# Performance work log

Hardware: AMD Instinct MI355X
Metric: run time of the kernel (lower is better)

Reference implementation:

```python
import jax, jax.numpy as jnp
import numpy as np

B, C, H, W = 8, 16, 512, 512


def setup_inputs() -> dict:
    key = jax.random.key(0)
    k1, k2, k3 = jax.random.split(key, 3)
    v = jax.random.normal(k1, (B, C, H, W), dtype=jnp.float32)
    # query coords in pixel units, slightly outside [0, W) / [0, H) to hit the invalid mask
    xq = jax.random.uniform(k2, (B, H, W), dtype=jnp.float32) * (W + 2.0) - 1.0
    yq = jax.random.uniform(k3, (B, H, W), dtype=jnp.float32) * (H + 2.0) - 1.0
    return {"v": v, "xq": xq, "yq": yq}


def reference(v, xq, yq):
    b, c, h, w = v.shape
    x0 = jnp.clip(jnp.floor(xq).astype(jnp.int32), 0, w - 1)
    y0 = jnp.clip(jnp.floor(yq).astype(jnp.int32), 0, h - 1)
    x1 = jnp.clip(x0 + 1, 0, w - 1)
    y1 = jnp.clip(y0 + 1, 0, h - 1)

    # flatten v to (B*H*W, C) like _bchw2bhwc(...).view(-1, C)
    v_flat = jnp.transpose(v, (0, 2, 3, 1)).reshape(-1, c)
    offs = (jnp.arange(b, dtype=jnp.int32) * (h * w))[:, None, None]  # [B,1,1]

    def gather(ys, xs):
        idx = (ys * w + xs + offs).reshape(-1)
        return jnp.take(v_flat, idx, axis=0).reshape(b, h, w, c)

    v00 = gather(y0, x0)
    v01 = gather(y0, x1)
    v10 = gather(y1, x0)
    v11 = gather(y1, x1)

    dx = xq - x0.astype(xq.dtype)  # [B,H,W]
    dy = yq - y0.astype(yq.dtype)
    w00 = ((1.0 - dy) * (1.0 - dx))[..., None]
    w01 = ((1.0 - dy) * dx)[..., None]
    w10 = (dy * (1.0 - dx))[..., None]
    w11 = (dy * dx)[..., None]

    out_bhwc = v00 * w00 + v01 * w01 + v10 * w10 + v11 * w11  # [B,H,W,C]
    values = jnp.transpose(out_bhwc, (0, 3, 1, 2))  # [B,C,H,W]

    invalid = ((xq < 0) | (xq >= w) | (yq < 0) | (yq >= h))[:, None, :, :]
    inv = invalid.astype(values.dtype)
    return inv * jnp.zeros_like(values) + (1.0 - inv) * values
```

## Files before the change

kernel.cpp:

```cpp
#include <hip/hip_runtime.h>
#include <hip/hip_fp16.h>


#define BATCH 8
#define CHAN  16
#define HEIGHT 512
#define WIDTH  512
#define HW (HEIGHT * WIDTH)
#define BLOCKS_PER_BATCH (HW / 256)

__global__ __launch_bounds__(256) void transpose_split_f16(
    const float* __restrict__ v, __half* __restrict__ vt0, __half* __restrict__ vt1)
{
    const int blk = blockIdx.x;
    const int b = blk & 7;
    const int j = blk >> 3;
    const int p = j * 256 + threadIdx.x;
    const int tid = b * HW + p;

    const float* src = v + (size_t)b * CHAN * HW + p;

    __half2 d[8];
#pragma unroll
    for (int j2 = 0; j2 < 8; ++j2) {
        const float lo = __builtin_nontemporal_load(&src[(size_t)(2 * j2 + 0) * HW]);
        const float hi = __builtin_nontemporal_load(&src[(size_t)(2 * j2 + 1) * HW]);
        d[j2] = __floats2half2_rn(lo, hi);
    }

    *(uint4*)(vt0 + (size_t)tid * 8) = *(const uint4*)&d[0];
    *(uint4*)(vt1 + (size_t)tid * 8) = *(const uint4*)&d[4];
}

__global__ __launch_bounds__(256) void interp2_half8(
    const __half* __restrict__ vth,
    const float* __restrict__ xq,
    const float* __restrict__ yq,
    float* __restrict__ out,
    int c0)
{
    const int blk = blockIdx.x;
    const int b = blk & 7;
    const int j = blk >> 3;
    const int p = j * 256 + threadIdx.x;
    const int qidx = b * HW + p;

    const float xqv = __builtin_nontemporal_load(&xq[qidx]);
    const float yqv = __builtin_nontemporal_load(&yq[qidx]);

    const bool invalid = (xqv < 0.0f) | (xqv >= (float)WIDTH) |
                         (yqv < 0.0f) | (yqv >= (float)HEIGHT);

    int x0 = (int)floorf(xqv);
    int y0 = (int)floorf(yqv);
    x0 = min(max(x0, 0), WIDTH - 1);
    y0 = min(max(y0, 0), HEIGHT - 1);
    const int x1 = min(x0 + 1, WIDTH - 1);
    const int y1 = min(y0 + 1, HEIGHT - 1);

    const float dx = xqv - (float)x0;
    const float dy = yqv - (float)y0;

    float w00 = (1.0f - dy) * (1.0f - dx);
    float w01 = (1.0f - dy) * dx;
    float w10 = dy * (1.0f - dx);
    float w11 = dy * dx;
    if (invalid) { w00 = 0.0f; w01 = 0.0f; w10 = 0.0f; w11 = 0.0f; }

    const size_t bbase = (size_t)b * HW;

    float acc[8];
#pragma unroll
    for (int c = 0; c < 8; ++c) acc[c] = 0.0f;

    auto corner = [&](int y, int x, float w) {
        const uint4 a = *(const uint4*)(vth + (bbase + (size_t)y * WIDTH + x) * 8);
        const __half2* h = (const __half2*)&a;
#pragma unroll
        for (int k = 0; k < 4; ++k) {
            const float2 f = __half22float2(h[k]);
            acc[2 * k + 0] += w * f.x;
            acc[2 * k + 1] += w * f.y;
        }
    };

    corner(y0, x0, w00);
    corner(y0, x1, w01);
    corner(y1, x0, w10);
    corner(y1, x1, w11);

    const size_t obase = (size_t)b * CHAN * HW + (size_t)c0 * HW + p;
#pragma unroll
    for (int c = 0; c < 8; ++c)
        __builtin_nontemporal_store(acc[c], &out[obase + (size_t)c * HW]);
}

__global__ __launch_bounds__(256) void interp2_bchw(
    const float* __restrict__ v,
    const float* __restrict__ xq,
    const float* __restrict__ yq,
    float* __restrict__ out)
{
    const int tid = blockIdx.x * blockDim.x + threadIdx.x;
    if (tid >= BATCH * HW) return;

    const int b   = tid / HW;
    const int pix = tid - b * HW;

    const float xqv = xq[tid];
    const float yqv = yq[tid];
    const bool invalid = (xqv < 0.0f) | (xqv >= (float)WIDTH) |
                         (yqv < 0.0f) | (yqv >= (float)HEIGHT);

    int x0 = (int)floorf(xqv);
    int y0 = (int)floorf(yqv);
    x0 = min(max(x0, 0), WIDTH - 1);
    y0 = min(max(y0, 0), HEIGHT - 1);
    const int x1 = min(x0 + 1, WIDTH - 1);
    const int y1 = min(y0 + 1, HEIGHT - 1);

    const float dx = xqv - (float)x0;
    const float dy = yqv - (float)y0;
    float w00 = (1.0f - dy) * (1.0f - dx);
    float w01 = (1.0f - dy) * dx;
    float w10 = dy * (1.0f - dx);
    float w11 = dy * dx;
    if (invalid) { w00 = 0.0f; w01 = 0.0f; w10 = 0.0f; w11 = 0.0f; }

    const int off00 = y0 * WIDTH + x0;
    const int off01 = y0 * WIDTH + x1;
    const int off10 = y1 * WIDTH + x0;
    const int off11 = y1 * WIDTH + x1;

    const int vbase = b * CHAN * HW;
    const int obase = vbase + pix;
#pragma unroll
    for (int c = 0; c < CHAN; ++c) {
        const int cb = vbase + c * HW;
        out[obase + c * HW] = v[cb + off00] * w00 + v[cb + off01] * w01 +
                              v[cb + off10] * w10 + v[cb + off11] * w11;
    }
}

extern "C" void kernel_launch(void* const* d_in, const int* in_sizes, int n_in,
                              void* d_out, int out_size, void* d_ws, size_t ws_size,
                              hipStream_t stream) {
    const float* v  = (const float*)d_in[0];
    const float* xq = (const float*)d_in[1];
    const float* yq = (const float*)d_in[2];
    float* out = (float*)d_out;

    const int grid = BATCH * BLOCKS_PER_BATCH;
    const size_t half_bytes = (size_t)BATCH * HW * 8 * sizeof(__half);

    if (ws_size >= 2 * half_bytes) {
        __half* vt0 = (__half*)d_ws;
        __half* vt1 = (__half*)((char*)d_ws + half_bytes);
        transpose_split_f16<<<grid, 256, 0, stream>>>(v, vt0, vt1);
        interp2_half8<<<grid, 256, 0, stream>>>(vt0, xq, yq, out, 0);
        interp2_half8<<<grid, 256, 0, stream>>>(vt1, xq, yq, out, 8);
    } else {
        const int npix = BATCH * HW;
        interp2_bchw<<<(npix + 255) / 256, 256, 0, stream>>>(v, xq, yq, out);
    }
}
```

Measured before the change: 134.7 us.

## Split fp16 transposed volume into four 4-channel planes with paired-pixel row loads

The transposed fp16 copy is now split into four planes of 4 channels each (8 bytes per pixel) instead of two planes of 8 channels. Each interp kernel fetches the two horizontally adjacent pixels of a row with one 16-byte load, clamping the left x so the pair stays in bounds and picking the right halves with selects. This halves the number of gather loads per corner pair and shrinks the per-plane footprint so it caches better. In exchange there are four interp launches instead of two, and xq/yq and the weights are recomputed in each of them.

```diff
diff --git a/kernel.cpp b/kernel.cpp
--- a/kernel.cpp
+++ b/kernel.cpp
@@ -7,33 +7,44 @@
 #define HEIGHT 512
 #define WIDTH  512
 #define HW (HEIGHT * WIDTH)
+#define QCH 4
+#define NQ  4
+#define QELEMS ((size_t)BATCH * HW * QCH)
 #define BLOCKS_PER_BATCH (HW / 256)
 
-__global__ __launch_bounds__(256) void transpose_split_f16(
-    const float* __restrict__ v, __half* __restrict__ vt0, __half* __restrict__ vt1)
+typedef unsigned int u32;
+typedef __attribute__((ext_vector_type(4), aligned(8))) u32 u32x4a;
+
+__device__ __forceinline__ float2 h2_to_f2(u32 u) {
+    const __half2 h = __builtin_bit_cast(__half2, u);
+    return __half22float2(h);
+}
+
+__global__ __launch_bounds__(256) void transpose_quarters_f16(
+    const float* __restrict__ v, __half* __restrict__ vt)
 {
     const int blk = blockIdx.x;
     const int b = blk & 7;
-    const int j = blk >> 3;
-    const int p = j * 256 + threadIdx.x;
+    const int p = (blk >> 3) * 256 + threadIdx.x;
     const int tid = b * HW + p;
 
     const float* src = v + (size_t)b * CHAN * HW + p;
 
     __half2 d[8];
 #pragma unroll
-    for (int j2 = 0; j2 < 8; ++j2) {
-        const float lo = __builtin_nontemporal_load(&src[(size_t)(2 * j2 + 0) * HW]);
-        const float hi = __builtin_nontemporal_load(&src[(size_t)(2 * j2 + 1) * HW]);
-        d[j2] = __floats2half2_rn(lo, hi);
+    for (int j = 0; j < 8; ++j) {
+        const float lo = __builtin_nontemporal_load(&src[(size_t)(2 * j + 0) * HW]);
+        const float hi = __builtin_nontemporal_load(&src[(size_t)(2 * j + 1) * HW]);
+        d[j] = __floats2half2_rn(lo, hi);
     }
 
-    *(uint4*)(vt0 + (size_t)tid * 8) = *(const uint4*)&d[0];
-    *(uint4*)(vt1 + (size_t)tid * 8) = *(const uint4*)&d[4];
+#pragma unroll
+    for (int q = 0; q < NQ; ++q)
+        *(uint2*)(vt + q * QELEMS + (size_t)tid * QCH) = *(const uint2*)&d[2 * q];
 }
 
-__global__ __launch_bounds__(256) void interp2_half8(
-    const __half* __restrict__ vth,
+__global__ __launch_bounds__(256) void interp2_quarter(
+    const __half* __restrict__ vq,
     const float* __restrict__ xq,
     const float* __restrict__ yq,
     float* __restrict__ out,
@@ -41,8 +52,7 @@
 {
     const int blk = blockIdx.x;
     const int b = blk & 7;
-    const int j = blk >> 3;
-    const int p = j * 256 + threadIdx.x;
+    const int p = (blk >> 3) * 256 + threadIdx.x;
     const int qidx = b * HW + p;
 
     const float xqv = __builtin_nontemporal_load(&xq[qidx]);
@@ -55,7 +65,6 @@
     int y0 = (int)floorf(yqv);
     x0 = min(max(x0, 0), WIDTH - 1);
     y0 = min(max(y0, 0), HEIGHT - 1);
-    const int x1 = min(x0 + 1, WIDTH - 1);
     const int y1 = min(y0 + 1, HEIGHT - 1);
 
     const float dx = xqv - (float)x0;
@@ -67,31 +76,32 @@
     float w11 = dy * dx;
     if (invalid) { w00 = 0.0f; w01 = 0.0f; w10 = 0.0f; w11 = 0.0f; }
 
+    const int bx = min(x0, WIDTH - 2);
+    const bool xlo = (x0 == bx);
+
     const size_t bbase = (size_t)b * HW;
+    const u32x4a r0 = *(const u32x4a*)(vq + (bbase + (size_t)y0 * WIDTH + bx) * QCH);
+    const u32x4a r1 = *(const u32x4a*)(vq + (bbase + (size_t)y1 * WIDTH + bx) * QCH);
 
-    float acc[8];
-#pragma unroll
-    for (int c = 0; c < 8; ++c) acc[c] = 0.0f;
+    const u32 c00a = xlo ? r0.x : r0.z, c00b = xlo ? r0.y : r0.w;
+    const u32 c10a = xlo ? r1.x : r1.z, c10b = xlo ? r1.y : r1.w;
 
-    auto corner = [&](int y, int x, float w) {
-        const uint4 a = *(const uint4*)(vth + (bbase + (size_t)y * WIDTH + x) * 8);
-        const __half2* h = (const __half2*)&a;
-#pragma unroll
-        for (int k = 0; k < 4; ++k) {
-            const float2 f = __half22float2(h[k]);
-            acc[2 * k + 0] += w * f.x;
-            acc[2 * k + 1] += w * f.y;
-        }
-    };
-
-    corner(y0, x0, w00);
-    corner(y0, x1, w01);
-    corner(y1, x0, w10);
-    corner(y1, x1, w11);
+    float acc[QCH];
+    {
+        float2 f;
+        f = h2_to_f2(c00a); acc[0]  = w00 * f.x; acc[1]  = w00 * f.y;
+        f = h2_to_f2(c00b); acc[2]  = w00 * f.x; acc[3]  = w00 * f.y;
+        f = h2_to_f2(r0.z); acc[0] += w01 * f.x; acc[1] += w01 * f.y;
+        f = h2_to_f2(r0.w); acc[2] += w01 * f.x; acc[3] += w01 * f.y;
+        f = h2_to_f2(c10a); acc[0] += w10 * f.x; acc[1] += w10 * f.y;
+        f = h2_to_f2(c10b); acc[2] += w10 * f.x; acc[3] += w10 * f.y;
+        f = h2_to_f2(r1.z); acc[0] += w11 * f.x; acc[1] += w11 * f.y;
+        f = h2_to_f2(r1.w); acc[2] += w11 * f.x; acc[3] += w11 * f.y;
+    }
 
     const size_t obase = (size_t)b * CHAN * HW + (size_t)c0 * HW + p;
 #pragma unroll
-    for (int c = 0; c < 8; ++c)
+    for (int c = 0; c < QCH; ++c)
         __builtin_nontemporal_store(acc[c], &out[obase + (size_t)c * HW]);
 }
 
@@ -151,14 +161,14 @@
     float* out = (float*)d_out;
 
     const int grid = BATCH * BLOCKS_PER_BATCH;
-    const size_t half_bytes = (size_t)BATCH * HW * 8 * sizeof(__half);
+    const size_t vt_bytes = NQ * QELEMS * sizeof(__half);
 
-    if (ws_size >= 2 * half_bytes) {
-        __half* vt0 = (__half*)d_ws;
-        __half* vt1 = (__half*)((char*)d_ws + half_bytes);
-        transpose_split_f16<<<grid, 256, 0, stream>>>(v, vt0, vt1);
-        interp2_half8<<<grid, 256, 0, stream>>>(vt0, xq, yq, out, 0);
-        interp2_half8<<<grid, 256, 0, stream>>>(vt1, xq, yq, out, 8);
+    if (ws_size >= vt_bytes) {
+        __half* vt = (__half*)d_ws;
+        transpose_quarters_f16<<<grid, 256, 0, stream>>>(v, vt);
+#pragma unroll
+        for (int q = 0; q < NQ; ++q)
+            interp2_quarter<<<grid, 256, 0, stream>>>(vt + q * QELEMS, xq, yq, out, q * QCH);
     } else {
         const int npix = BATCH * HW;
         interp2_bchw<<<(npix + 255) / 256, 256, 0, stream>>>(v, xq, yq, out);
```

Result: slower. 144.6 us (+7.3%).
